# Performance work log

Measured on AMD Instinct MI355X. Metric: run time of the kernel, lower is better.

Reference implementation:

```python
import jax, jax.numpy as jnp
import numpy as np
from jax import lax

TAU = 1.0
GUMBEL_SCALE = 1e-4
SEARCH_SPACE = [1, 2, 4, 8, 16, 32, 64]


def synth_weight(weight, alphas_after):
    """Per-block circulant projection of weight for each block size, mixed by alphas.

    weight: [O, I, k, k]. For block size b: reshape to (q,b,p,b,k,k), rotate rows so
    each circulant diagonal aligns, mean over the block row axis, broadcast back with
    the reverse rotation, and accumulate alpha-weighted.
    """
    O, I, k, _ = weight.shape
    w = alphas_after[0] * weight  # block_size == 1 -> identity
    for idx, b in enumerate(SEARCH_SPACE[1:], start=1):
        q, p = O // b, I // b
        tmp = weight.reshape(q, b, p, b, k, k).transpose(0, 2, 1, 3, 4, 5)  # q,p,b,b,k,k
        ii = jnp.arange(b)[:, None]
        jj = jnp.arange(b)[None, :]
        rot = tmp[:, :, ii, (ii + jj) % b]          # q,p,b,b,k,k : rotate_mat gather
        cir = rot.mean(axis=2)                       # q,p,b,k,k   : circulant mean
        out = cir[:, :, (jj - ii) % b]               # q,p,b,b,k,k : rev_rotate_mat gather
        out = out.transpose(0, 2, 1, 3, 4, 5).reshape(O, I, k, k)
        w = w + alphas_after[idx] * out
    return w


def setup_inputs() -> dict:
    key = jax.random.key(0)
    k1, k2, k3 = jax.random.split(key, 3)
    B, C, H = 16, 256, 56
    O, I, K = 256, 256, 3
    x = jax.random.normal(k1, (B, C, H, H), dtype=jnp.float32)
    # kaiming-uniform-ish init: uniform in [-bound, bound], bound = sqrt(6/fan_in)
    fan_in = I * K * K
    bound = float(np.sqrt(6.0 / fan_in))
    weight = jax.random.uniform(k2, (O, I, K, K), dtype=jnp.float32, minval=-bound, maxval=bound)
    alphas = jnp.ones((len(SEARCH_SPACE),), dtype=jnp.float32)
    gumbels = jax.random.normal(k3, (len(SEARCH_SPACE),), dtype=jnp.float32)
    return {"x": x, "weight": weight, "alphas": alphas, "gumbels": gumbels}


def reference(x, weight, alphas, gumbels):
    # gumbel_softmax with tiny Gumbel(0, 1e-4) noise (noise passed in for determinism)
    alphas_after = jax.nn.softmax((alphas + GUMBEL_SCALE * gumbels) / TAU, axis=-1)
    w = synth_weight(weight, alphas_after)
    k = weight.shape[-1]
    pad = k // 2
    stride = 1
    out = lax.conv_general_dilated(
        x, w,
        window_strides=(stride, stride),
        padding=[(pad, pad), (pad, pad)],
        dimension_numbers=("NCHW", "OIHW", "NCHW"),
    )
    return out
```

## Files before the change

kernel.cpp:

```cpp
#include <hip/hip_runtime.h>
#include <hip/hip_bf16.h>

typedef __attribute__((ext_vector_type(8))) short bf16x8;
typedef __attribute__((ext_vector_type(4))) float f32x4;

#define WR_OFF   27557888

#define BAND 24576

__global__ void diagsum_kernel(const float* __restrict__ W, float* __restrict__ S) {
    int t = blockIdx.x * 256 + threadIdx.x;
    int idx, n, lvlOff;
    if (t < 32768)      { idx = 1; n = t;          lvlOff = 0; }
    else if (t < 49152) { idx = 2; n = t - 32768;  lvlOff = 294912; }
    else if (t < 57344) { idx = 3; n = t - 49152;  lvlOff = 442368; }
    else if (t < 61440) { idx = 4; n = t - 57344;  lvlOff = 516096; }
    else if (t < 63488) { idx = 5; n = t - 61440;  lvlOff = 552960; }
    else                { idx = 6; n = t - 63488;  lvlOff = 571392; }
    int b = 1 << idx;
    int d = n & (b - 1);
    int qp = n >> idx;
    int p = qp & ((256 >> idx) - 1);
    int q = qp >> (8 - idx);
    float s[9];
    #pragma unroll
    for (int tp = 0; tp < 9; ++tp) s[tp] = 0.f;
    for (int tt = 0; tt < b; ++tt) {
        const float* wp = W + ((size_t)((q * b + tt) * 256 + p * b + ((tt + d) & (b - 1)))) * 9;
        #pragma unroll
        for (int tp = 0; tp < 9; ++tp) s[tp] += wp[tp];
    }
    float* o = S + (size_t)lvlOff + (size_t)n * 9;
    #pragma unroll
    for (int tp = 0; tp < 9; ++tp) o[tp] = s[tp];
}

__global__ void wsynth_kernel(const float* __restrict__ W,
                              const float* __restrict__ alphas,
                              const float* __restrict__ gumbels,
                              const float* __restrict__ S,
                              __hip_bfloat16* __restrict__ Wr) {
    int tid = blockIdx.x * 256 + threadIdx.x;
    int o = tid >> 8, i = tid & 255;

    float a[7]; float mx = -1e30f;
    for (int j = 0; j < 7; ++j) { a[j] = alphas[j] + 1.0e-4f * gumbels[j]; mx = fmaxf(mx, a[j]); }
    float s = 0.f;
    for (int j = 0; j < 7; ++j) { a[j] = __expf(a[j] - mx); s += a[j]; }
    float invs = 1.0f / s;
    for (int j = 0; j < 7; ++j) a[j] *= invs;

    float acc[9];
    const float* w0 = W + ((size_t)(o * 256 + i)) * 9;
    #pragma unroll
    for (int t = 0; t < 9; ++t) acc[t] = a[0] * w0[t];

    const int lvlOff[7] = {0, 0, 294912, 442368, 516096, 552960, 571392};
    int dif = i - o;
    #pragma unroll
    for (int idx = 1; idx < 7; ++idx) {
        int b = 1 << idx;
        int q = o >> idx, p = i >> idx, d = dif & (b - 1);
        int n = ((q * (256 >> idx) + p) << idx) + d;
        const float* sp = S + lvlOff[idx] + (size_t)n * 9;
        float sc = a[idx] / (float)b;
        #pragma unroll
        for (int tp = 0; tp < 9; ++tp) acc[tp] += sc * sp[tp];
    }
    const size_t eb = (size_t)(i >> 5) * 8192 + ((i >> 3) & 3) * 2048 + o * 8 + (i & 7);
    #pragma unroll
    for (int tp = 0; tp < 9; ++tp)
        Wr[(size_t)tp * 65536 + eb] = __float2bfloat16(acc[tp]);
}

__global__ void pad_nhwc_kernel(const float* __restrict__ x,
                                __hip_bfloat16* __restrict__ Xp) {
    {
        int bl = (blockIdx.z * 4 + blockIdx.y) * 49 + blockIdx.x;
        int L = bl * 256 + threadIdx.x;
        for (int e = L; e < 933888; e += 802816) {
            int c = e & 255;
            int pp = e >> 8;
            int b = pp / 228;
            int p = pp - b * 228;
            int y, xx;
            if (p < 58)       { y = 0;             xx = p; }
            else if (p < 116) { y = 57;            xx = p - 58; }
            else if (p < 172) { y = 1 + (p - 116); xx = 0; }
            else              { y = 1 + (p - 172); xx = 57; }
            Xp[((size_t)(b * 58 + y) * 58 + xx) * 256 + c] = __float2bfloat16(0.f);
        }
    }
    __shared__ float t[64][65];
    int p0 = blockIdx.x * 64;
    int c0 = blockIdx.y * 64;
    int b  = blockIdx.z;
    int lane = threadIdx.x & 63;
    int grp  = threadIdx.x >> 6;

    const float* src = x + ((size_t)(b * 256 + c0)) * 3136 + p0;
    #pragma unroll
    for (int it = 0; it < 16; ++it) {
        int c = it * 4 + grp;
        t[c][lane] = src[(size_t)c * 3136 + lane];
    }
    __syncthreads();
    #pragma unroll
    for (int it = 0; it < 16; ++it) {
        int pl = it * 4 + grp;
        int P = p0 + pl;
        int y = P / 56, xx = P - y * 56;
        Xp[(((size_t)(b * 58 + y + 1)) * 58 + (xx + 1)) * 256 + c0 + lane] =
            __float2bfloat16(t[lane][pl]);
    }
}

__device__ __forceinline__ void gload16(const __hip_bfloat16* g, char* l) {
    __builtin_amdgcn_global_load_lds(
        (const __attribute__((address_space(1))) void*)g,
        (__attribute__((address_space(3))) void*)l, 16, 0, 0);
}

template<int N> __device__ __forceinline__ void gate() {
    if constexpr (N == 0)      asm volatile("s_waitcnt vmcnt(0)" ::: "memory");
    else if constexpr (N == 4) asm volatile("s_waitcnt vmcnt(4)" ::: "memory");
}

template<bool LAST>
__device__ __forceinline__ void chunk_pair(
    int cp, char* smem, const char* aBase,
    const int (&bOff)[7], const __hip_bfloat16* const (&xSrc)[3],
    int tid, bf16x8 (&afr)[2][4], f32x4 (&acc)[4][7])
{
    #pragma unroll
    for (int u = 0; u < 2; ++u) {
        const int cc = 2 * cp + u;
        const char* xb = smem + u * BAND;
        #pragma unroll
        for (int r = 0; r < 9; ++r) {
            const int cur = (u + r) & 1, nxt = cur ^ 1;
            if (!(LAST && u == 1 && r == 8)) {
                const int tapn = (r == 8) ? 0 : r + 1;
                const int aoff = tapn * 131072 + (cc + (r == 8 ? 1 : 0)) * 16384;
                #pragma unroll
                for (int nf = 0; nf < 4; ++nf)
                    afr[nxt][nf] = *(const bf16x8*)(aBase + aoff + nf * 256);
            }
            if (!(LAST && u == 1) && r == 3) {
                char* d = smem + (u ^ 1) * BAND + tid * 16;
                #pragma unroll
                for (int it = 0; it < 3; ++it)
                    gload16(xSrc[it] + (cc + 1) * 32, d + it * 8192);
            }
            const int dy = r / 3 - 1, dx = r % 3 - 1;
            const int timm = (dy * 64 + dx) * 16;
            bf16x8 bfv[7];
            #pragma unroll
            for (int mf = 0; mf < 7; ++mf)
                bfv[mf] = *(const bf16x8*)(xb + bOff[mf] + timm);
            __builtin_amdgcn_s_setprio(1);
            #pragma unroll
            for (int nf = 0; nf < 4; ++nf)
                #pragma unroll
                for (int mf = 0; mf < 7; ++mf)
                    acc[nf][mf] = __builtin_amdgcn_mfma_f32_16x16x32_bf16(
                        afr[cur][nf], bfv[mf], acc[nf][mf], 0, 0, 0);
            __builtin_amdgcn_s_setprio(0);
            if (r == 8 && !(LAST && u == 1)) {
                gate<4>();
                __builtin_amdgcn_s_barrier();
            }
        }
    }
}

__global__ __launch_bounds__(512, 2) void conv_kernel(
        const __hip_bfloat16* __restrict__ Xp,
        const __hip_bfloat16* __restrict__ Wr,
        float* __restrict__ out) {
    __shared__ char smem[2 * BAND];

    const int tid = threadIdx.x;
    const int w = tid >> 6, lane = tid & 63, l15 = lane & 15, q = lane >> 4;
    const int bid = blockIdx.x;
    const int bimg = bid / 14;
    const int y0 = (bid - bimg * 14) * 4;

    const int wn = (w & 3) << 6;
    const int wm = (w >> 2) * 112;

    const char* aBase = (const char*)Wr + q * 4096 + (wn + l15) * 16;

    const __hip_bfloat16* xSrc[3];
    #pragma unroll
    for (int it = 0; it < 3; ++it) {
        int chunk = tid + it * 512;
        int slot = chunk / 384;
        int rem  = chunk - slot * 384;
        int row = rem >> 6, xcol = rem & 63;
        xSrc[it] = Xp + (((size_t)(bimg * 58 + y0 + row)) * 58 + xcol) * 256 + slot * 8;
    }

    int bOff[7];
    #pragma unroll
    for (int mf = 0; mf < 7; ++mf) {
        int p = wm + mf * 16 + l15;
        int y = p / 56, xx = p - y * 56;
        bOff[mf] = q * 6144 + ((y + 1) * 64 + (xx + 1)) * 16;
    }

    f32x4 acc[4][7];
    #pragma unroll
    for (int a1 = 0; a1 < 4; ++a1)
        #pragma unroll
        for (int a2 = 0; a2 < 7; ++a2)
            acc[a1][a2] = (f32x4){0.f, 0.f, 0.f, 0.f};

    bf16x8 afr[2][4];

    {
        char* d = smem + tid * 16;
        #pragma unroll
        for (int it = 0; it < 3; ++it) gload16(xSrc[it], d + it * 8192);
    }
    #pragma unroll
    for (int nf = 0; nf < 4; ++nf)
        afr[0][nf] = *(const bf16x8*)(aBase + nf * 256);
    gate<0>();
    __builtin_amdgcn_s_barrier();

    for (int cp = 0; cp < 3; ++cp)
        chunk_pair<false>(cp, smem, aBase, bOff, xSrc, tid, afr, acc);
    chunk_pair<true>(3, smem, aBase, bOff, xSrc, tid, afr, acc);

    const int nb = wn + q * 4;
    const size_t obB = (size_t)bimg * 256 * 3136;
    #pragma unroll
    for (int mf = 0; mf < 7; ++mf) {
        int pm = y0 * 56 + wm + mf * 16 + l15;
        #pragma unroll
        for (int nf = 0; nf < 4; ++nf) {
            #pragma unroll
            for (int rr = 0; rr < 4; ++rr)
                out[obB + (size_t)(nb + nf * 16 + rr) * 3136 + pm] = acc[nf][mf][rr];
        }
    }
}

extern "C" void kernel_launch(void* const* d_in, const int* in_sizes, int n_in,
                              void* d_out, int out_size, void* d_ws, size_t ws_size,
                              hipStream_t stream) {
    const float* x       = (const float*)d_in[0];
    const float* weight  = (const float*)d_in[1];
    const float* alphas  = (const float*)d_in[2];
    const float* gumbels = (const float*)d_in[3];
    float* out = (float*)d_out;

    __hip_bfloat16* Xp = (__hip_bfloat16*)d_ws;
    float*          S  = (float*)d_ws;
    __hip_bfloat16* Wr = (__hip_bfloat16*)((char*)d_ws + WR_OFF);

    hipLaunchKernelGGL(diagsum_kernel,  dim3(252),       dim3(256), 0, stream,
                       weight, S);
    hipLaunchKernelGGL(wsynth_kernel,   dim3(256),       dim3(256), 0, stream,
                       weight, alphas, gumbels, S, Wr);
    hipLaunchKernelGGL(pad_nhwc_kernel, dim3(49, 4, 16), dim3(256), 0, stream,
                       x, Xp);
    hipLaunchKernelGGL(conv_kernel,     dim3(224),       dim3(512), 0, stream,
                       Xp, Wr, out);
}
```

Before: 96.74 us.

## Double-buffer LDS B fragments and issue next-chunk global loads earlier

Each tap's B-operand LDS reads are now prefetched one step ahead into a double-buffered register array, so the MFMA block of a tap no longer waits on its own LDS reads. The prefetch for the next chunk's first tap comes from the other LDS buffer. To make that possible, the async global-to-LDS copy of the next chunk moves to the start of the chunk, and the wait-plus-barrier moves one tap earlier. A sched_barrier keeps the loads ahead of the MFMAs. The cost is more live VGPRs, which risks spills or lower occupancy under the 512x2 launch bounds, and tighter ordering between LDS reuse and the barrier.

```diff
diff --git a/kernel.cpp b/kernel.cpp
--- a/kernel.cpp
+++ b/kernel.cpp
@@ -130,7 +130,7 @@
 __device__ __forceinline__ void chunk_pair(
     int cp, char* smem, const char* aBase,
     const int (&bOff)[7], const __hip_bfloat16* const (&xSrc)[3],
-    int tid, bf16x8 (&afr)[2][4], f32x4 (&acc)[4][7])
+    int tid, bf16x8 (&afr)[2][4], bf16x8 (&bfv)[2][7], f32x4 (&acc)[4][7])
 {
     #pragma unroll
     for (int u = 0; u < 2; ++u) {
@@ -139,6 +139,12 @@
         #pragma unroll
         for (int r = 0; r < 9; ++r) {
             const int cur = (u + r) & 1, nxt = cur ^ 1;
+            if (r == 0 && !(LAST && u == 1)) {
+                char* d = smem + (u ^ 1) * BAND + tid * 16;
+                #pragma unroll
+                for (int it = 0; it < 3; ++it)
+                    gload16(xSrc[it] + (cc + 1) * 32, d + it * 8192);
+            }
             if (!(LAST && u == 1 && r == 8)) {
                 const int tapn = (r == 8) ? 0 : r + 1;
                 const int aoff = tapn * 131072 + (cc + (r == 8 ? 1 : 0)) * 16384;
@@ -146,27 +152,29 @@
                 for (int nf = 0; nf < 4; ++nf)
                     afr[nxt][nf] = *(const bf16x8*)(aBase + aoff + nf * 256);
             }
-            if (!(LAST && u == 1) && r == 3) {
-                char* d = smem + (u ^ 1) * BAND + tid * 16;
-                #pragma unroll
-                for (int it = 0; it < 3; ++it)
-                    gload16(xSrc[it] + (cc + 1) * 32, d + it * 8192);
-            }
-            const int dy = r / 3 - 1, dx = r % 3 - 1;
-            const int timm = (dy * 64 + dx) * 16;
-            bf16x8 bfv[7];
-            #pragma unroll
-            for (int mf = 0; mf < 7; ++mf)
-                bfv[mf] = *(const bf16x8*)(xb + bOff[mf] + timm);
+            if (r < 8) {
+                const int tapn = r + 1;
+                const int timn = ((tapn / 3 - 1) * 64 + (tapn % 3 - 1)) * 16;
+                #pragma unroll
+                for (int mf = 0; mf < 7; ++mf)
+                    bfv[nxt][mf] = *(const bf16x8*)(xb + bOff[mf] + timn);
+            } else if (!(LAST && u == 1)) {
+                const int timn = (-64 - 1) * 16;
+                const char* xb2 = smem + (u ^ 1) * BAND;
+                #pragma unroll
+                for (int mf = 0; mf < 7; ++mf)
+                    bfv[nxt][mf] = *(const bf16x8*)(xb2 + bOff[mf] + timn);
+            }
+            __builtin_amdgcn_sched_barrier(0);
             __builtin_amdgcn_s_setprio(1);
             #pragma unroll
             for (int nf = 0; nf < 4; ++nf)
                 #pragma unroll
                 for (int mf = 0; mf < 7; ++mf)
                     acc[nf][mf] = __builtin_amdgcn_mfma_f32_16x16x32_bf16(
-                        afr[cur][nf], bfv[mf], acc[nf][mf], 0, 0, 0);
+                        afr[cur][nf], bfv[cur][mf], acc[nf][mf], 0, 0, 0);
             __builtin_amdgcn_s_setprio(0);
-            if (r == 8 && !(LAST && u == 1)) {
+            if (r == 7 && !(LAST && u == 1)) {
                 gate<4>();
                 __builtin_amdgcn_s_barrier();
             }
@@ -216,7 +224,7 @@
         for (int a2 = 0; a2 < 7; ++a2)
             acc[a1][a2] = (f32x4){0.f, 0.f, 0.f, 0.f};
 
-    bf16x8 afr[2][4];
+    bf16x8 afr[2][4], bfv[2][7];
 
     {
         char* d = smem + tid * 16;
@@ -228,10 +236,16 @@
         afr[0][nf] = *(const bf16x8*)(aBase + nf * 256);
     gate<0>();
     __builtin_amdgcn_s_barrier();
+    {
+        const int timm = (-64 - 1) * 16;
+        #pragma unroll
+        for (int mf = 0; mf < 7; ++mf)
+            bfv[0][mf] = *(const bf16x8*)(smem + bOff[mf] + timm);
+    }
 
     for (int cp = 0; cp < 3; ++cp)
-        chunk_pair<false>(cp, smem, aBase, bOff, xSrc, tid, afr, acc);
-    chunk_pair<true>(3, smem, aBase, bOff, xSrc, tid, afr, acc);
+        chunk_pair<false>(cp, smem, aBase, bOff, xSrc, tid, afr, bfv, acc);
+    chunk_pair<true>(3, smem, aBase, bOff, xSrc, tid, afr, bfv, acc);
 
     const int nb = wn + q * 4;
     const size_t obB = (size_t)bimg * 256 * 3136;
```

New measurement: 96.57 us. About the same (-0.2%).

## Split conv output channels across two blocks and simplify per-chunk pipeline

Applied to the files above, without the earlier changes.

The conv kernel now splits the 256 output channels into two halves handled by separate blocks, doubling the grid to 448 blocks and halving per-wave accumulators (2x7 tiles instead of 4x7). Launch bounds rise to 4 blocks per CU to exploit the lower register use. The hand-tuned A-fragment double buffering and vmcnt gating are dropped in favour of direct loads per tap and __syncthreads. This improves occupancy and fills more CUs, at the cost of loading each input tile twice and losing explicit prefetch overlap.

```diff
diff --git a/kernel.cpp b/kernel.cpp
--- a/kernel.cpp
+++ b/kernel.cpp
@@ -121,60 +121,42 @@
         (__attribute__((address_space(3))) void*)l, 16, 0, 0);
 }
 
-template<int N> __device__ __forceinline__ void gate() {
-    if constexpr (N == 0)      asm volatile("s_waitcnt vmcnt(0)" ::: "memory");
-    else if constexpr (N == 4) asm volatile("s_waitcnt vmcnt(4)" ::: "memory");
-}
-
 template<bool LAST>
-__device__ __forceinline__ void chunk_pair(
-    int cp, char* smem, const char* aBase,
+__device__ __forceinline__ void chunk_body(
+    int cc, char* smem, const char* aBase,
     const int (&bOff)[7], const __hip_bfloat16* const (&xSrc)[3],
-    int tid, bf16x8 (&afr)[2][4], f32x4 (&acc)[4][7])
+    int tid, f32x4 (&acc)[2][7])
 {
-    #pragma unroll
-    for (int u = 0; u < 2; ++u) {
-        const int cc = 2 * cp + u;
-        const char* xb = smem + u * BAND;
-        #pragma unroll
-        for (int r = 0; r < 9; ++r) {
-            const int cur = (u + r) & 1, nxt = cur ^ 1;
-            if (!(LAST && u == 1 && r == 8)) {
-                const int tapn = (r == 8) ? 0 : r + 1;
-                const int aoff = tapn * 131072 + (cc + (r == 8 ? 1 : 0)) * 16384;
-                #pragma unroll
-                for (int nf = 0; nf < 4; ++nf)
-                    afr[nxt][nf] = *(const bf16x8*)(aBase + aoff + nf * 256);
-            }
-            if (!(LAST && u == 1) && r == 3) {
-                char* d = smem + (u ^ 1) * BAND + tid * 16;
-                #pragma unroll
-                for (int it = 0; it < 3; ++it)
-                    gload16(xSrc[it] + (cc + 1) * 32, d + it * 8192);
-            }
-            const int dy = r / 3 - 1, dx = r % 3 - 1;
-            const int timm = (dy * 64 + dx) * 16;
-            bf16x8 bfv[7];
+    const char* xb = smem + (cc & 1) * BAND;
+    #pragma unroll
+    for (int r = 0; r < 9; ++r) {
+        const int aoff = r * 131072 + cc * 16384;
+        bf16x8 af0 = *(const bf16x8*)(aBase + aoff);
+        bf16x8 af1 = *(const bf16x8*)(aBase + aoff + 256);
+        if (!LAST && r == 3) {
+            char* d = smem + ((cc + 1) & 1) * BAND + tid * 16;
             #pragma unroll
-            for (int mf = 0; mf < 7; ++mf)
-                bfv[mf] = *(const bf16x8*)(xb + bOff[mf] + timm);
-            __builtin_amdgcn_s_setprio(1);
-            #pragma unroll
-            for (int nf = 0; nf < 4; ++nf)
-                #pragma unroll
-                for (int mf = 0; mf < 7; ++mf)
-                    acc[nf][mf] = __builtin_amdgcn_mfma_f32_16x16x32_bf16(
-                        afr[cur][nf], bfv[mf], acc[nf][mf], 0, 0, 0);
-            __builtin_amdgcn_s_setprio(0);
-            if (r == 8 && !(LAST && u == 1)) {
-                gate<4>();
-                __builtin_amdgcn_s_barrier();
-            }
-        }
-    }
-}
-
-__global__ __launch_bounds__(512, 2) void conv_kernel(
+            for (int it = 0; it < 3; ++it)
+                gload16(xSrc[it] + (cc + 1) * 32, d + it * 8192);
+        }
+        const int dy = r / 3 - 1, dx = r % 3 - 1;
+        const int timm = (dy * 64 + dx) * 16;
+        bf16x8 bfv[7];
+        #pragma unroll
+        for (int mf = 0; mf < 7; ++mf)
+            bfv[mf] = *(const bf16x8*)(xb + bOff[mf] + timm);
+        __builtin_amdgcn_s_setprio(1);
+        #pragma unroll
+        for (int mf = 0; mf < 7; ++mf) {
+            acc[0][mf] = __builtin_amdgcn_mfma_f32_16x16x32_bf16(af0, bfv[mf], acc[0][mf], 0, 0, 0);
+            acc[1][mf] = __builtin_amdgcn_mfma_f32_16x16x32_bf16(af1, bfv[mf], acc[1][mf], 0, 0, 0);
+        }
+        __builtin_amdgcn_s_setprio(0);
+        if (r == 8 && !LAST) __syncthreads();
+    }
+}
+
+__global__ __launch_bounds__(512, 4) void conv_kernel(
         const __hip_bfloat16* __restrict__ Xp,
         const __hip_bfloat16* __restrict__ Wr,
         float* __restrict__ out) {
@@ -183,13 +165,15 @@
     const int tid = threadIdx.x;
     const int w = tid >> 6, lane = tid & 63, l15 = lane & 15, q = lane >> 4;
     const int bid = blockIdx.x;
-    const int bimg = bid / 14;
-    const int y0 = (bid - bimg * 14) * 4;
-
-    const int wn = (w & 3) << 6;
+    const int mt  = bid % 224;
+    const int n0  = (bid / 224) * 128;
+    const int bimg = mt / 14;
+    const int y0 = (mt - bimg * 14) * 4;
+
+    const int wn = (w & 3) << 5;
     const int wm = (w >> 2) * 112;
 
-    const char* aBase = (const char*)Wr + q * 4096 + (wn + l15) * 16;
+    const char* aBase = (const char*)Wr + q * 4096 + (n0 + wn + l15) * 16;
 
     const __hip_bfloat16* xSrc[3];
     #pragma unroll
@@ -209,37 +193,31 @@
         bOff[mf] = q * 6144 + ((y + 1) * 64 + (xx + 1)) * 16;
     }
 
-    f32x4 acc[4][7];
-    #pragma unroll
-    for (int a1 = 0; a1 < 4; ++a1)
+    f32x4 acc[2][7];
+    #pragma unroll
+    for (int a1 = 0; a1 < 2; ++a1)
         #pragma unroll
         for (int a2 = 0; a2 < 7; ++a2)
             acc[a1][a2] = (f32x4){0.f, 0.f, 0.f, 0.f};
 
-    bf16x8 afr[2][4];
-
     {
         char* d = smem + tid * 16;
         #pragma unroll
         for (int it = 0; it < 3; ++it) gload16(xSrc[it], d + it * 8192);
     }
-    #pragma unroll
-    for (int nf = 0; nf < 4; ++nf)
-        afr[0][nf] = *(const bf16x8*)(aBase + nf * 256);
-    gate<0>();
-    __builtin_amdgcn_s_barrier();
-
-    for (int cp = 0; cp < 3; ++cp)
-        chunk_pair<false>(cp, smem, aBase, bOff, xSrc, tid, afr, acc);
-    chunk_pair<true>(3, smem, aBase, bOff, xSrc, tid, afr, acc);
-
-    const int nb = wn + q * 4;
+    __syncthreads();
+
+    for (int cc = 0; cc < 7; ++cc)
+        chunk_body<false>(cc, smem, aBase, bOff, xSrc, tid, acc);
+    chunk_body<true>(7, smem, aBase, bOff, xSrc, tid, acc);
+
+    const int nb = n0 + wn + q * 4;
     const size_t obB = (size_t)bimg * 256 * 3136;
     #pragma unroll
     for (int mf = 0; mf < 7; ++mf) {
         int pm = y0 * 56 + wm + mf * 16 + l15;
         #pragma unroll
-        for (int nf = 0; nf < 4; ++nf) {
+        for (int nf = 0; nf < 2; ++nf) {
             #pragma unroll
             for (int rr = 0; rr < 4; ++rr)
                 out[obB + (size_t)(nb + nf * 16 + rr) * 3136 + pm] = acc[nf][mf][rr];
@@ -266,6 +244,6 @@
                        weight, alphas, gumbels, S, Wr);
     hipLaunchKernelGGL(pad_nhwc_kernel, dim3(49, 4, 16), dim3(256), 0, stream,
                        x, Xp);
-    hipLaunchKernelGGL(conv_kernel,     dim3(224),       dim3(512), 0, stream,
+    hipLaunchKernelGGL(conv_kernel,     dim3(448),       dim3(512), 0, stream,
                        Xp, Wr, out);
 }
```

Result: slower. 102.4 us (+5.8%).
